# Kernel optimization log

Hardware: AMD Instinct MI355X
Metric: run time of the kernel (lower is better)

The kernel has to match this reference:

```python
import jax, jax.numpy as jnp
import numpy as np

N = 256
BATCH = 32768
FROZEN_POS = np.arange(128)                      # rate-1/2 code, k = 128
FROZEN_IND = np.zeros(N, dtype=bool)
FROZEN_IND[FROZEN_POS] = True
INFO_POS = np.setdiff1d(np.arange(N), FROZEN_POS)
LLR_MAX = 30.0


def _cn_op(x, y):
    # f-function. Original clips then (for all modes, due to the unconditional
    # overwrite in the torch code) applies min-sum: sign(x)*sign(y)*min(|x|,|y|).
    xc = jnp.clip(x, -LLR_MAX, LLR_MAX)
    yc = jnp.clip(y, -LLR_MAX, LLR_MAX)
    return jnp.sign(xc) * jnpp_sign(yc) if False else jnp.sign(xc) * jnp.sign(yc) * jnp.minimum(jnp.abs(xc), jnp.abs(yc))


def _sc_decode(llr, frozen):
    """Recursive SC decode over a contiguous sub-block.

    llr:    [bs, m] channel-side LLRs at this stage.
    frozen: numpy bool [m], static at trace time (recursion unrolls under jit).
    Returns (u_leaf [bs, m] leaf bit decisions, x [bs, m] partial-sum bits).
    """
    m = llr.shape[-1]
    if m == 1:
        if frozen[0]:
            u = jnp.zeros_like(llr)
        else:
            # u = 0.5*(1-sign(llr)), ties (llr==0 -> 0.5) mapped to 1  =>  (llr <= 0)
            u = (llr <= 0).astype(llr.dtype)
        return u, u
    h = m // 2
    ll, lr = llr[:, :h], llr[:, h:]
    u_left, x_left = _sc_decode(_cn_op(ll, lr), frozen[:h])
    # g-function (VN update): (1 - 2*u_hat) * x + y   (unclipped llrs, as in source)
    g = (1.0 - 2.0 * x_left) * ll + lr
    u_right, x_right = _sc_decode(g, frozen[h:])
    # combine partial sums: left XOR right on the left half, right passes through
    x = jnp.concatenate([(x_left != x_right).astype(llr.dtype), x_right], axis=-1)
    return jnp.concatenate([u_left, u_right], axis=-1), x


def setup_inputs() -> dict:
    key = jax.random.key(0)
    inputs = jax.random.normal(key, (BATCH, N), dtype=jnp.float32)
    return {"inputs": inputs}


def reference(inputs):
    llr_ch = -1.0 * inputs.astype(jnp.float32)   # [bs, n]
    u_hat, _ = _sc_decode(llr_ch, FROZEN_IND)    # stage-0 leaf decisions
    return u_hat[..., INFO_POS]                  # [bs, k]
```

## Files before the change

### kernel.cpp

```cpp
#include <hip/hip_runtime.h>
#include <stdint.h>

__global__ __launch_bounds__(256) void sc_dec_kernel(const float* __restrict__ in,
                                                     float* __restrict__ out,
                                                     int rows) {
    const int lane = threadIdx.x & 63;
    const int waves_per_block = blockDim.x >> 6;
    int wave = blockIdx.x * waves_per_block + (threadIdx.x >> 6);
    const int nwaves = gridDim.x * waves_per_block;

    for (int row = wave; row < rows; row += nwaves) {
        const float2* rin = reinterpret_cast<const float2*>(in + (size_t)row * 256);
        float2 a = rin[lane];
        float2 c = rin[64 + lane];

        float s0 = a.x + c.x;
        float s1 = a.y + c.y;
        unsigned long long B0 = __ballot(s0 >= 0.0f);
        unsigned long long B1 = __ballot(s1 >= 0.0f);

        unsigned long long w0 = B0 ^ B1;
        unsigned long long w1 = B1;
        w0 ^= w0 >> 32;                                  w1 ^= w1 >> 32;
        w0 ^= (w0 >> 16) & 0x0000FFFF0000FFFFull;        w1 ^= (w1 >> 16) & 0x0000FFFF0000FFFFull;
        w0 ^= (w0 >> 8)  & 0x00FF00FF00FF00FFull;        w1 ^= (w1 >> 8)  & 0x00FF00FF00FF00FFull;
        w0 ^= (w0 >> 4)  & 0x0F0F0F0F0F0F0F0Full;        w1 ^= (w1 >> 4)  & 0x0F0F0F0F0F0F0F0Full;
        w0 ^= (w0 >> 2)  & 0x3333333333333333ull;        w1 ^= (w1 >> 2)  & 0x3333333333333333ull;
        w0 ^= (w0 >> 1)  & 0x5555555555555555ull;        w1 ^= (w1 >> 1)  & 0x5555555555555555ull;

        float2 o;
        o.x = (float)((w0 >> lane) & 1ull);
        o.y = (float)((w1 >> lane) & 1ull);
        reinterpret_cast<float2*>(out + (size_t)row * 128)[lane] = o;
    }
}

extern "C" void kernel_launch(void* const* d_in, const int* in_sizes, int n_in,
                              void* d_out, int out_size, void* d_ws, size_t ws_size,
                              hipStream_t stream) {
    const float* in = (const float*)d_in[0];
    float* out = (float*)d_out;
    const int rows = in_sizes[0] / 256;

    const int threads = 256;
    int blocks = 2048;
    int max_blocks = (rows + 3) / 4;
    if (blocks > max_blocks) blocks = max_blocks;
    if (blocks < 1) blocks = 1;

    sc_dec_kernel<<<blocks, threads, 0, stream>>>(in, out, rows);
}
```

Measured before the change: 13.37 us.

## Process four rows per wave with 16-byte nontemporal loads and one-shot grid

Each wave now handles four rows at once: two rows per 128-bit vector load pair, with lanes split into halves that each own one row. Ballots over the four float components are recombined into per-row bitmasks before the XOR butterfly. All accesses become 16-byte nontemporal loads and stores, and the grid-stride loop is replaced by a grid sized to cover all rows once. This cuts instruction count and per-row loop overhead and widens memory transactions, in exchange for more complex bit-shuffling and a scalar fallback for tail rows.

New measurement: 12.35 us. 7.6% less time.

```diff
diff --git a/kernel.cpp b/kernel.cpp
--- a/kernel.cpp
+++ b/kernel.cpp
@@ -1,37 +1,96 @@
 #include <hip/hip_runtime.h>
 #include <stdint.h>
+
+typedef unsigned long long u64;
+typedef float f32x4 __attribute__((ext_vector_type(4)));
+
+
+__device__ __forceinline__ void butterfly128(u64& w0, u64& w1) {
+    w0 ^= w1;
+    w0 ^= w0 >> 32;                              w1 ^= w1 >> 32;
+    w0 ^= (w0 >> 16) & 0x0000FFFF0000FFFFull;    w1 ^= (w1 >> 16) & 0x0000FFFF0000FFFFull;
+    w0 ^= (w0 >> 8)  & 0x00FF00FF00FF00FFull;    w1 ^= (w1 >> 8)  & 0x00FF00FF00FF00FFull;
+    w0 ^= (w0 >> 4)  & 0x0F0F0F0F0F0F0F0Full;    w1 ^= (w1 >> 4)  & 0x0F0F0F0F0F0F0F0Full;
+    w0 ^= (w0 >> 2)  & 0x3333333333333333ull;    w1 ^= (w1 >> 2)  & 0x3333333333333333ull;
+    w0 ^= (w0 >> 1)  & 0x5555555555555555ull;    w1 ^= (w1 >> 1)  & 0x5555555555555555ull;
+}
+
+__device__ __forceinline__ void pair_masks(const f32x4& A, const f32x4& B,
+                                           u64& wa0, u64& wa1, u64& wb0, u64& wb1) {
+    u64 M0 = __ballot(A.x + B.x >= 0.0f);
+    u64 M1 = __ballot(A.y + B.y >= 0.0f);
+    u64 M2 = __ballot(A.z + B.z >= 0.0f);
+    u64 M3 = __ballot(A.w + B.w >= 0.0f);
+    wa0 = (M0 & 0xFFFFFFFFull) | (M1 << 32);
+    wa1 = (M2 & 0xFFFFFFFFull) | (M3 << 32);
+    wb0 = (M0 >> 32) | (M1 & 0xFFFFFFFF00000000ull);
+    wb1 = (M2 >> 32) | (M3 & 0xFFFFFFFF00000000ull);
+}
 
 __global__ __launch_bounds__(256) void sc_dec_kernel(const float* __restrict__ in,
                                                      float* __restrict__ out,
                                                      int rows) {
     const int lane = threadIdx.x & 63;
-    const int waves_per_block = blockDim.x >> 6;
-    int wave = blockIdx.x * waves_per_block + (threadIdx.x >> 6);
-    const int nwaves = gridDim.x * waves_per_block;
+    const int h = lane >> 5;
+    const int m = lane & 31;
+    const int wave = blockIdx.x * (blockDim.x >> 6) + (threadIdx.x >> 6);
+    const int r = wave * 4;
+    if (r >= rows) return;
 
-    for (int row = wave; row < rows; row += nwaves) {
-        const float2* rin = reinterpret_cast<const float2*>(in + (size_t)row * 256);
-        float2 a = rin[lane];
-        float2 c = rin[64 + lane];
+    if (r + 4 <= rows) {
+        const f32x4* b0 = reinterpret_cast<const f32x4*>(in + (size_t)r * 256);
+        const f32x4* b1 = reinterpret_cast<const f32x4*>(in + (size_t)(r + 2) * 256);
+        const int oA = (h << 6) + m;
+        const int oB = oA + 32;
+        f32x4 A0 = __builtin_nontemporal_load(&b0[oA]);
+        f32x4 B0 = __builtin_nontemporal_load(&b0[oB]);
+        f32x4 A1 = __builtin_nontemporal_load(&b1[oA]);
+        f32x4 B1 = __builtin_nontemporal_load(&b1[oB]);
 
-        float s0 = a.x + c.x;
-        float s1 = a.y + c.y;
-        unsigned long long B0 = __ballot(s0 >= 0.0f);
-        unsigned long long B1 = __ballot(s1 >= 0.0f);
+        u64 a0, a1, c0, c1;
+        pair_masks(A0, B0, a0, a1, c0, c1);
+        butterfly128(a0, a1);
+        butterfly128(c0, c1);
+        u64 w0 = h ? c0 : a0, w1 = h ? c1 : a1;
+        f32x4 o;
+        o.x = (float)((w0 >> m) & 1ull);
+        o.y = (float)((w0 >> (m + 32)) & 1ull);
+        o.z = (float)((w1 >> m) & 1ull);
+        o.w = (float)((w1 >> (m + 32)) & 1ull);
+        f32x4* ob0 = reinterpret_cast<f32x4*>(out + (size_t)r * 128);
+        __builtin_nontemporal_store(o, &ob0[(h << 5) + m]);
 
-        unsigned long long w0 = B0 ^ B1;
-        unsigned long long w1 = B1;
-        w0 ^= w0 >> 32;                                  w1 ^= w1 >> 32;
-        w0 ^= (w0 >> 16) & 0x0000FFFF0000FFFFull;        w1 ^= (w1 >> 16) & 0x0000FFFF0000FFFFull;
-        w0 ^= (w0 >> 8)  & 0x00FF00FF00FF00FFull;        w1 ^= (w1 >> 8)  & 0x00FF00FF00FF00FFull;
-        w0 ^= (w0 >> 4)  & 0x0F0F0F0F0F0F0F0Full;        w1 ^= (w1 >> 4)  & 0x0F0F0F0F0F0F0F0Full;
-        w0 ^= (w0 >> 2)  & 0x3333333333333333ull;        w1 ^= (w1 >> 2)  & 0x3333333333333333ull;
-        w0 ^= (w0 >> 1)  & 0x5555555555555555ull;        w1 ^= (w1 >> 1)  & 0x5555555555555555ull;
-
-        float2 o;
-        o.x = (float)((w0 >> lane) & 1ull);
-        o.y = (float)((w1 >> lane) & 1ull);
-        reinterpret_cast<float2*>(out + (size_t)row * 128)[lane] = o;
+        pair_masks(A1, B1, a0, a1, c0, c1);
+        butterfly128(a0, a1);
+        butterfly128(c0, c1);
+        w0 = h ? c0 : a0; w1 = h ? c1 : a1;
+        o.x = (float)((w0 >> m) & 1ull);
+        o.y = (float)((w0 >> (m + 32)) & 1ull);
+        o.z = (float)((w1 >> m) & 1ull);
+        o.w = (float)((w1 >> (m + 32)) & 1ull);
+        f32x4* ob1 = reinterpret_cast<f32x4*>(out + (size_t)(r + 2) * 128);
+        __builtin_nontemporal_store(o, &ob1[(h << 5) + m]);
+    } else {
+        for (int row = r; row < rows; ++row) {
+            const float2* rin = reinterpret_cast<const float2*>(in + (size_t)row * 256);
+            float2 a = rin[lane];
+            float2 c = rin[64 + lane];
+            u64 B0 = __ballot(a.x + c.x >= 0.0f);
+            u64 B1 = __ballot(a.y + c.y >= 0.0f);
+            u64 w0 = B0;
+            u64 w1 = B1;
+            w0 ^= w1;
+            w0 ^= w0 >> 32;                              w1 ^= w1 >> 32;
+            w0 ^= (w0 >> 16) & 0x0000FFFF0000FFFFull;    w1 ^= (w1 >> 16) & 0x0000FFFF0000FFFFull;
+            w0 ^= (w0 >> 8)  & 0x00FF00FF00FF00FFull;    w1 ^= (w1 >> 8)  & 0x00FF00FF00FF00FFull;
+            w0 ^= (w0 >> 4)  & 0x0F0F0F0F0F0F0F0Full;    w1 ^= (w1 >> 4)  & 0x0F0F0F0F0F0F0F0Full;
+            w0 ^= (w0 >> 2)  & 0x3333333333333333ull;    w1 ^= (w1 >> 2)  & 0x3333333333333333ull;
+            w0 ^= (w0 >> 1)  & 0x5555555555555555ull;    w1 ^= (w1 >> 1)  & 0x5555555555555555ull;
+            float2 o;
+            o.x = (float)((w0 >> lane) & 1ull);
+            o.y = (float)((w1 >> lane) & 1ull);
+            reinterpret_cast<float2*>(out + (size_t)row * 128)[lane] = o;
+        }
     }
 }
 
@@ -42,11 +101,7 @@
     float* out = (float*)d_out;
     const int rows = in_sizes[0] / 256;
 
-    const int threads = 256;
-    int blocks = 2048;
-    int max_blocks = (rows + 3) / 4;
-    if (blocks > max_blocks) blocks = max_blocks;
-    if (blocks < 1) blocks = 1;
-
-    sc_dec_kernel<<<blocks, threads, 0, stream>>>(in, out, rows);
+    const int waves = (rows + 3) / 4;
+    const int blocks = (waves + 3) / 4;
+    sc_dec_kernel<<<blocks, 256, 0, stream>>>(in, out, rows);
 }
```
